# Kernel optimization log

Measured on AMD Instinct MI355X. Metric: run time of the kernel, lower is better.

## Reference

```python
import jax, jax.numpy as jnp
import numpy as np


def setup_inputs() -> dict:
    key = jax.random.key(0)
    ks = jax.random.split(key, 7)
    B, T, C, D = 8, 2048, 1024, 128
    x = jax.random.normal(ks[0], (B, T, C), dtype=jnp.float32)
    # torch nn.Linear weights are [out_features, in_features]
    s = 1.0 / np.sqrt(C)
    Wq = jax.random.normal(ks[1], (D, C), dtype=jnp.float32) * s
    bq = jax.random.normal(ks[2], (D,), dtype=jnp.float32) * s
    Wk = jax.random.normal(ks[3], (D, C), dtype=jnp.float32) * s
    bk = jax.random.normal(ks[4], (D,), dtype=jnp.float32) * s
    Wv = jax.random.normal(ks[5], (D, C), dtype=jnp.float32) * s
    bv = jax.random.normal(ks[6], (D,), dtype=jnp.float32) * s
    return {"x": x, "Wq": Wq, "bq": bq, "Wk": Wk, "bk": bk, "Wv": Wv, "bv": bv}


def reference(x, Wq, bq, Wk, bk, Wv, bv):
    B, T, C = x.shape
    q = jnp.einsum('btc,dc->btd', x, Wq) + bq  # [B,T,D]
    k = jnp.einsum('btc,dc->btd', x, Wk) + bk
    v = jnp.einsum('btc,dc->btd', x, Wv) + bv
    scores = jnp.einsum('btd,bsd->bts', q, k)  # [B,T,T]
    causal = jnp.tril(jnp.ones((T, T), dtype=bool))
    masked = jnp.where(causal, scores, -jnp.inf)
    # NOTE: original scales by sqrt(key.weight.shape[-1]) == sqrt(emb_dim), AFTER masking
    scale = jnp.asarray(C, dtype=x.dtype) ** 0.5
    attn = jax.nn.softmax(masked / scale, axis=-1)
    return jnp.einsum('bts,bsd->btd', attn, v)
```

## Files before the change

kernel.cpp:

```cpp
#include <hip/hip_runtime.h>
#include <hip/hip_bf16.h>
#include <math.h>

typedef __bf16 bf16_t;
typedef __bf16 bf16x4 __attribute__((ext_vector_type(4)));
typedef __bf16 bf16x8 __attribute__((ext_vector_type(8)));
typedef float  f32x4  __attribute__((ext_vector_type(4)));
typedef float  f32x16 __attribute__((ext_vector_type(16)));
typedef int    v2i    __attribute__((ext_vector_type(2)));

static constexpr int Bz = 8, Tt = 2048, Cc = 1024, Dd = 128;
static constexpr int Mm = Bz * Tt;
static constexpr int NT128 = Tt / 128;

__device__ __forceinline__ bf16x8 lds_read8(const char* base, int byte) {
    return *(const bf16x8*)(base + byte);
}

__device__ __forceinline__ bf16x8 cvt8(float4 a, float4 b) {
    bf16x8 r;
    r[0] = (bf16_t)a.x; r[1] = (bf16_t)a.y; r[2] = (bf16_t)a.z; r[3] = (bf16_t)a.w;
    r[4] = (bf16_t)b.x; r[5] = (bf16_t)b.y; r[6] = (bf16_t)b.z; r[7] = (bf16_t)b.w;
    return r;
}

__device__ __forceinline__ unsigned cvtpk(float lo, float hi) {
    unsigned r;
    asm("v_cvt_pk_bf16_f32 %0, %1, %2" : "=v"(r) : "v"(lo), "v"(hi));
    return r;
}

__global__ __launch_bounds__(256) void wcvt_kernel(
    const float* __restrict__ Wq, const float* __restrict__ Wk,
    const float* __restrict__ Wv, bf16_t* __restrict__ Wp)
{
    int g = (blockIdx.x * 256 + threadIdx.x) * 4;
    int n = g >> 10;
    int k = g & 1023;
    int sel = n >> 7;
    const float* W = (sel == 0) ? Wq : (sel == 1) ? Wk : Wv;
    float4 f = *(const float4*)(W + (size_t)(n & 127) * 1024 + k);
    bf16x4 o; o[0] = (bf16_t)f.x; o[1] = (bf16_t)f.y; o[2] = (bf16_t)f.z; o[3] = (bf16_t)f.w;
    int ktile = k >> 6, kk = (k >> 5) & 1, hi = (k >> 3) & 3, e = k & 7;
    int addr = (((((ktile * 24 + (n >> 4)) * 2 + kk) * 4 + hi) * 16 + (n & 15)) * 8) + e;
    *(bf16x4*)(Wp + addr) = o;
}

__global__ __launch_bounds__(256) void qkv_fused(
    const float* __restrict__ x, const bf16_t* __restrict__ Wp,
    const float* __restrict__ bq, const float* __restrict__ bk, const float* __restrict__ bv,
    bf16_t* __restrict__ qo, bf16_t* __restrict__ ko, bf16_t* __restrict__ vTo)
{
    const int m0   = blockIdx.x * 32;
    const int tid  = threadIdx.x;
    const int lane = tid & 63;
    const int w    = tid >> 6;
    const int lo   = lane & 15;
    const int hi   = lane >> 4;

    __shared__ bf16_t Xs[2][32 * 64];

    f32x4 zero4 = {0.f, 0.f, 0.f, 0.f};
    f32x4 acc[2][6];
    #pragma unroll
    for (int i = 0; i < 2; i++)
        #pragma unroll
        for (int j = 0; j < 6; j++) acc[i][j] = zero4;

    const int xrow = tid >> 3;
    const int xcol = (tid & 7) * 8;

    float4 fx[2];
    auto load_x = [&](int k0) {
        const float4* s = (const float4*)(x + (size_t)(m0 + xrow) * Cc + k0 + xcol);
        fx[0] = s[0]; fx[1] = s[1];
    };
    auto write_x = [&](int buf) {
        int byte = (xrow * 128 + xcol * 2) ^ ((xrow & 7) << 4);
        *(bf16x8*)((char*)Xs[buf] + byte) = cvt8(fx[0], fx[1]);
    };

    bf16x8 bfrA[2][6], bfrB[2][6];
    auto loadB = [&](bf16x8 (&dst)[2][6], int k0) {
        const bf16_t* base = Wp + (size_t)(k0 >> 6) * (24 * 2 * 64 * 8) + lane * 8;
        #pragma unroll
        for (int j = 0; j < 6; j++)
            #pragma unroll
            for (int kk = 0; kk < 2; kk++)
                dst[kk][j] = *(const bf16x8*)(base + (((w * 6 + j) * 2 + kk) * 64) * 8);
    };
    auto mfma_step = [&](const bf16x8 (&bfr)[2][6], int buf) {
        #pragma unroll
        for (int kk = 0; kk < 2; kk++) {
            bf16x8 af0 = lds_read8((char*)Xs[buf], ((lo)      * 128 + kk * 64 + hi * 16) ^ ((lo & 7) << 4));
            bf16x8 af1 = lds_read8((char*)Xs[buf], ((16 + lo) * 128 + kk * 64 + hi * 16) ^ ((lo & 7) << 4));
            #pragma unroll
            for (int j = 0; j < 6; j++)
                acc[0][j] = __builtin_amdgcn_mfma_f32_16x16x32_bf16(af0, bfr[kk][j], acc[0][j], 0, 0, 0);
            #pragma unroll
            for (int j = 0; j < 6; j++)
                acc[1][j] = __builtin_amdgcn_mfma_f32_16x16x32_bf16(af1, bfr[kk][j], acc[1][j], 0, 0, 0);
        }
    };

    load_x(0); write_x(0); loadB(bfrA, 0);
    __syncthreads();
    load_x(64); loadB(bfrB, 64);

    for (int k0 = 0; k0 < Cc; k0 += 128) {
        const bool m2 = (k0 + 128 < Cc);
        mfma_step(bfrA, 0);
        write_x(1);
        if (m2) load_x(k0 + 128);
        __syncthreads();
        if (m2) loadB(bfrA, k0 + 128);
        mfma_step(bfrB, 1);
        if (m2) { write_x(0); load_x(k0 + 192); }
        __syncthreads();
        if (k0 + 192 < Cc) loadB(bfrB, k0 + 192);
    }

    #pragma unroll
    for (int j = 0; j < 6; j++) {
        int c = w * 96 + j * 16 + lo;
        int t = c >> 7, d = c & 127;
        const float* bp = (t == 0) ? bq : (t == 1) ? bk : bv;
        float bb = bp[d];
        #pragma unroll
        for (int i = 0; i < 2; i++)
            #pragma unroll
            for (int r = 0; r < 4; r++) {
                int m = m0 + i * 16 + hi * 4 + r;
                float v = acc[i][j][r] + bb;
                if (t == 0)      qo[(size_t)m * Dd + d] = (bf16_t)v;
                else if (t == 1) ko[(size_t)m * Dd + d] = (bf16_t)v;
                else             vTo[(size_t)d * Mm + m] = (bf16_t)v;
            }
    }
}

__global__ __launch_bounds__(256, 2) void attn_kernel(
    const bf16_t* __restrict__ qi, const bf16_t* __restrict__ ki,
    const bf16_t* __restrict__ vTi,
    float* __restrict__ Opart, float* __restrict__ Mpart, float* __restrict__ Lpart,
    int nsplit)
{
    const int g   = blockIdx.x;
    const int per = nsplit * 8;
    const int qt  = (NT128 - 1) - g / per;
    const int rem = g % per;
    const int s   = rem >> 3;
    const int b   = rem & 7;
    const int nt  = 2 * qt + 2;
    const int t_lo = (s * nt) / nsplit;
    const int t_hi = ((s + 1) * nt) / nsplit;

    const int q0   = qt * 128;
    const int tid  = threadIdx.x;
    const int lane = tid & 63;
    const int w    = tid >> 6;
    const int rq   = lane & 31;
    const int dh   = lane >> 5;

    float* Ob = Opart + ((size_t)s * Mm + (size_t)b * Tt + q0) * Dd;
    float* Mb = Mpart + (size_t)s * Mm + (size_t)b * Tt + q0;
    float* Lb = Lpart + (size_t)s * Mm + (size_t)b * Tt + q0;

    if (t_lo >= t_hi) {
        float4 z = {0.f, 0.f, 0.f, 0.f};
        #pragma unroll
        for (int i = 0; i < 16; i++)
            ((float4*)Ob)[i * 256 + tid] = z;
        if (tid < 128) { Mb[tid] = -INFINITY; Lb[tid] = 0.f; }
        return;
    }

    __shared__ __align__(16) char smem[65536];

    const float SCALE = 1.4426950408889634f / 32.0f;
    const int qg = q0 + w * 32 + rq;
    const int qwmax = q0 + w * 32 + 31;

    bf16x8 qf[8];
    {
        const bf16_t* qrow = qi + (size_t)(b * Tt + qg) * Dd;
        #pragma unroll
        for (int ks = 0; ks < 8; ks++)
            qf[ks] = *(const bf16x8*)(qrow + ks * 16 + dh * 8);
    }

    f32x16 accO[4];
    #pragma unroll
    for (int ds = 0; ds < 4; ds++)
        #pragma unroll
        for (int e = 0; e < 16; e++) accO[ds][e] = 0.f;
    float mrun = -INFINITY, lrun = 0.f;

    const int krow = tid >> 2;
    const int kcol = (tid & 3) * 32;
    const int vrow = tid >> 1;
    const int vcol = (tid & 1) * 32;

    bf16x8 kr[4], vr[4];
    auto load_kv = [&](int t) {
        const int kv0 = t * 64;
        const bf16_t* ksrc = ki + (size_t)(b * Tt + kv0 + krow) * Dd + kcol;
        #pragma unroll
        for (int i = 0; i < 4; i++) kr[i] = *(const bf16x8*)(ksrc + i * 8);
        const bf16_t* vsrc = vTi + (size_t)vrow * Mm + (b * Tt + kv0 + vcol);
        #pragma unroll
        for (int i = 0; i < 4; i++) vr[i] = *(const bf16x8*)(vsrc + i * 8);
    };
    auto write_kv = [&](int buf) {
        char* Ksb = smem + buf * 16384;
        char* Vsb = smem + 32768 + buf * 16384;
        #pragma unroll
        for (int i = 0; i < 4; i++) {
            int byte = (krow * 256 + (kcol + i * 8) * 2) ^ ((krow & 15) << 4);
            *(bf16x8*)(Ksb + byte) = kr[i];
        }
        const int vlr = vrow & 63;
        const int vlc = (vrow >> 6) * 64 + vcol;
        #pragma unroll
        for (int i = 0; i < 4; i++) {
            int byte = (vlr * 256 + (vlc + i * 8) * 2) ^ ((vlr & 15) << 4);
            *(bf16x8*)(Vsb + byte) = vr[i];
        }
    };

    load_kv(t_lo);
    write_kv(0);
    int buf = 0;

    for (int t = t_lo; t < t_hi; t++) {
        const int kv0 = t * 64;
        const bool more = (t + 1 < t_hi);
        __syncthreads();
        if (more) load_kv(t + 1);

        if (kv0 <= qwmax) {
            const char* Ksb = smem + buf * 16384;
            const char* Vsb = smem + 32768 + buf * 16384;

            f32x16 accS0, accS1;
            #pragma unroll
            for (int e = 0; e < 16; e++) { accS0[e] = 0.f; accS1[e] = 0.f; }
            #pragma unroll
            for (int ks = 0; ks < 8; ks++) {
                int colb = (ks * 16 + dh * 8) * 2;
                bf16x8 kf0 = lds_read8(Ksb, ((rq)      * 256 + colb) ^ ((rq & 15) << 4));
                bf16x8 kf1 = lds_read8(Ksb, ((32 + rq) * 256 + colb) ^ ((rq & 15) << 4));
                accS0 = __builtin_amdgcn_mfma_f32_32x32x16_bf16(kf0, qf[ks], accS0, 0, 0, 0);
                accS1 = __builtin_amdgcn_mfma_f32_32x32x16_bf16(kf1, qf[ks], accS1, 0, 0, 0);
            }

            float pl[32];
            #pragma unroll
            for (int e = 0; e < 16; e++) {
                pl[e]      = accS0[e] * SCALE;
                pl[16 + e] = accS1[e] * SCALE;
            }
            if (kv0 + 63 > qg) {
                #pragma unroll
                for (int e = 0; e < 16; e++) {
                    int kg = kv0 + 8 * (e >> 2) + (e & 3) + 4 * dh;
                    if (kg > qg)      pl[e]      = -INFINITY;
                    if (kg + 32 > qg) pl[16 + e] = -INFINITY;
                }
            }

            float mt = pl[0];
            #pragma unroll
            for (int e = 1; e < 32; e++) mt = fmaxf(mt, pl[e]);
            mt = fmaxf(mt, __shfl_xor(mt, 32, 64));
            float mnew = fmaxf(mrun, mt);
            float muse = (mnew == -INFINITY) ? 0.f : mnew;
            float alpha = exp2f(mrun - muse);
            mrun = mnew;
            float ps = 0.f;
            #pragma unroll
            for (int e = 0; e < 32; e++) {
                float pv = exp2f(pl[e] - muse);
                pl[e] = pv;
                ps += pv;
            }
            lrun = alpha * lrun + ps;
            #pragma unroll
            for (int ds = 0; ds < 4; ds++)
                #pragma unroll
                for (int e = 0; e < 16; e++) accO[ds][e] *= alpha;

            unsigned u0[8], u1[8];
            #pragma unroll
            for (int gg = 0; gg < 8; gg++) {
                u0[gg] = cvtpk(pl[4 * gg + 0], pl[4 * gg + 1]);
                u1[gg] = cvtpk(pl[4 * gg + 2], pl[4 * gg + 3]);
            }
            bf16x8 pa[4];
            #pragma unroll
            for (int ks = 0; ks < 4; ks++) {
                v2i rA = __builtin_amdgcn_permlane32_swap((int)u0[2 * ks], (int)u0[2 * ks + 1], false, false);
                v2i rB = __builtin_amdgcn_permlane32_swap((int)u1[2 * ks], (int)u1[2 * ks + 1], false, false);
                union { unsigned wd[4]; bf16x8 v; } pu;
                pu.wd[0] = (unsigned)rA[0];
                pu.wd[1] = (unsigned)rB[0];
                pu.wd[2] = (unsigned)rA[1];
                pu.wd[3] = (unsigned)rB[1];
                pa[ks] = pu.v;
            }

            #pragma unroll
            for (int ds = 0; ds < 4; ds++) {
                int row  = (ds & 1) * 32 + rq;
                int cb   = (ds >> 1) * 64;
                #pragma unroll
                for (int ks = 0; ks < 4; ks++) {
                    int colb = (cb + ks * 16 + dh * 8) * 2;
                    bf16x8 vf = lds_read8(Vsb, (row * 256 + colb) ^ ((row & 15) << 4));
                    accO[ds] = __builtin_amdgcn_mfma_f32_32x32x16_bf16(vf, pa[ks], accO[ds], 0, 0, 0);
                }
            }
        }

        __syncthreads();
        if (more) write_kv(buf ^ 1);
        buf ^= 1;
    }

    __syncthreads();

    lrun += __shfl_xor(lrun, 32, 64);

    char* slab = smem + w * 8192;
    #pragma unroll
    for (int half = 0; half < 2; half++) {
        #pragma unroll
        for (int dsl = 0; dsl < 2; dsl++) {
            #pragma unroll
            for (int e = 0; e < 16; e++) {
                int d = 8 * (e >> 2) + (e & 3) + 4 * dh + 32 * dsl;
                int byte = (rq * 256 + d * 4) ^ ((rq & 15) << 4);
                *(float*)(slab + byte) = accO[half * 2 + dsl][e];
            }
        }
        __builtin_amdgcn_s_waitcnt(0);
        #pragma unroll
        for (int i = 0; i < 8; i++) {
            int dd = 32 * dh + 4 * i;
            int byte = (rq * 256 + dd * 4) ^ ((rq & 15) << 4);
            float4 val = *(float4*)(slab + byte);
            *(float4*)(Ob + (size_t)(w * 32 + rq) * Dd + half * 64 + dd) = val;
        }
        __builtin_amdgcn_s_waitcnt(0);
    }

    if (lane < 32) {
        Mb[w * 32 + rq] = mrun;
        Lb[w * 32 + rq] = lrun;
    }
}

__global__ __launch_bounds__(256) void combine_kernel(
    const float* __restrict__ Opart, const float* __restrict__ Mpart,
    const float* __restrict__ Lpart, float* __restrict__ out, int nsplit)
{
    int t   = blockIdx.x * 256 + threadIdx.x;
    int row = t >> 5;
    int dq  = (t & 31) << 2;
    float M = -INFINITY;
    for (int s = 0; s < nsplit; s++)
        M = fmaxf(M, Mpart[(size_t)s * Mm + row]);
    float L = 0.f;
    float o0 = 0.f, o1 = 0.f, o2 = 0.f, o3 = 0.f;
    for (int s = 0; s < nsplit; s++) {
        float ms = Mpart[(size_t)s * Mm + row];
        float ws = (ms == -INFINITY) ? 0.f : exp2f(ms - M);
        L += ws * Lpart[(size_t)s * Mm + row];
        float4 p = *(const float4*)(Opart + ((size_t)s * Mm + row) * Dd + dq);
        o0 += ws * p.x; o1 += ws * p.y; o2 += ws * p.z; o3 += ws * p.w;
    }
    float inv = 1.0f / L;
    float4 r; r.x = o0 * inv; r.y = o1 * inv; r.z = o2 * inv; r.w = o3 * inv;
    *(float4*)(out + (size_t)row * Dd + dq) = r;
}

extern "C" void kernel_launch(void* const* d_in, const int* in_sizes, int n_in,
                              void* d_out, int out_size, void* d_ws, size_t ws_size,
                              hipStream_t stream)
{
    const float* x  = (const float*)d_in[0];
    const float* Wq = (const float*)d_in[1];
    const float* bq = (const float*)d_in[2];
    const float* Wk = (const float*)d_in[3];
    const float* bk = (const float*)d_in[4];
    const float* Wv = (const float*)d_in[5];
    const float* bv = (const float*)d_in[6];
    float* out = (float*)d_out;

    bf16_t* qb = (bf16_t*)d_ws;
    bf16_t* kb = qb + (size_t)Mm * Dd;
    bf16_t* vT = kb + (size_t)Mm * Dd;
    bf16_t* Wp = vT + (size_t)Mm * Dd;
    char* p = (char*)(Wp + (size_t)384 * Cc);

    auto need = [&](int ns) {
        return (size_t)3 * Mm * Dd * 2 + (size_t)384 * Cc * 2
             + (size_t)ns * Mm * Dd * 4 + (size_t)ns * Mm * 8;
    };
    int nsplit = 4;
    while (nsplit > 1 && need(nsplit) > ws_size) nsplit >>= 1;

    float* Opart = (float*)p;
    float* Mpart = (float*)(p + (size_t)nsplit * Mm * Dd * 4);
    float* Lpart = Mpart + (size_t)nsplit * Mm;

    wcvt_kernel<<<dim3(384), 256, 0, stream>>>(Wq, Wk, Wv, Wp);
    qkv_fused<<<dim3(Mm / 32), 256, 0, stream>>>(x, Wp, bq, bk, bv, qb, kb, vT);
    attn_kernel<<<dim3(NT128 * nsplit * Bz), 256, 0, stream>>>(qb, kb, vT, Opart, Mpart, Lpart, nsplit);
    combine_kernel<<<dim3(Mm * 32 / 256), 256, 0, stream>>>(Opart, Mpart, Lpart, out, nsplit);
}
```

Measured before the change: 70.40 us.

## Retile QKV projection GEMM with LDS-staged weights via direct global-to-LDS loads

Restructures the QKV projection kernel: each block now covers 64 rows and half of the 384 output columns (2D grid, 512 threads), and it stages weight tiles into double-buffered LDS using global_load_lds. Previously every wave loaded its B fragments straight from global into registers. The weight packing layout changes to match the column-group split. This cuts redundant per-wave weight traffic and register pressure so that more rows share each weight load. The cost is more LDS use and a single sync per k-step, which could limit overlap.

```diff
diff --git a/kernel.cpp b/kernel.cpp
--- a/kernel.cpp
+++ b/kernel.cpp
@@ -28,6 +28,13 @@
     unsigned r;
     asm("v_cvt_pk_bf16_f32 %0, %1, %2" : "=v"(r) : "v"(lo), "v"(hi));
     return r;
+}
+
+typedef const __attribute__((address_space(1))) unsigned int* as1_u32p;
+typedef __attribute__((address_space(3))) unsigned int* as3_u32p;
+
+__device__ __forceinline__ void gload_lds16(const bf16_t* g, bf16_t* l) {
+    __builtin_amdgcn_global_load_lds((as1_u32p)(const void*)g, (as3_u32p)(void*)l, 16, 0, 0);
 }
 
 __global__ __launch_bounds__(256) void wcvt_kernel(
@@ -42,99 +49,97 @@
     float4 f = *(const float4*)(W + (size_t)(n & 127) * 1024 + k);
     bf16x4 o; o[0] = (bf16_t)f.x; o[1] = (bf16_t)f.y; o[2] = (bf16_t)f.z; o[3] = (bf16_t)f.w;
     int ktile = k >> 6, kk = (k >> 5) & 1, hi = (k >> 3) & 3, e = k & 7;
-    int addr = (((((ktile * 24 + (n >> 4)) * 2 + kk) * 4 + hi) * 16 + (n & 15)) * 8) + e;
+    int ng = n >> 4, cg = ng / 12, ngl = ng % 12, lo = n & 15;
+    size_t addr = (size_t)(((((ktile * 2 + cg) * 12 + ngl) * 2 + kk) * 4 + hi) * 16 + lo) * 8 + e;
     *(bf16x4*)(Wp + addr) = o;
 }
 
-__global__ __launch_bounds__(256) void qkv_fused(
+__global__ __launch_bounds__(512, 4) void qkv_fused(
     const float* __restrict__ x, const bf16_t* __restrict__ Wp,
     const float* __restrict__ bq, const float* __restrict__ bk, const float* __restrict__ bv,
     bf16_t* __restrict__ qo, bf16_t* __restrict__ ko, bf16_t* __restrict__ vTo)
 {
-    const int m0   = blockIdx.x * 32;
-    const int tid  = threadIdx.x;
+    const int m0  = blockIdx.x * 64;
+    const int cg  = blockIdx.y;
+    const int tid = threadIdx.x;
     const int lane = tid & 63;
-    const int w    = tid >> 6;
-    const int lo   = lane & 15;
-    const int hi   = lane >> 4;
-
-    __shared__ bf16_t Xs[2][32 * 64];
+    const int wv  = tid >> 6;
+    const int wr  = wv >> 2;
+    const int cw  = wv & 3;
+    const int lo  = lane & 15;
+    const int hi  = lane >> 4;
+
+    __shared__ bf16_t Wl[2][12 * 2 * 512];
+    __shared__ bf16_t Xs[2][64 * 64];
 
     f32x4 zero4 = {0.f, 0.f, 0.f, 0.f};
-    f32x4 acc[2][6];
+    f32x4 acc[2][3];
     #pragma unroll
     for (int i = 0; i < 2; i++)
         #pragma unroll
-        for (int j = 0; j < 6; j++) acc[i][j] = zero4;
+        for (int j = 0; j < 3; j++) acc[i][j] = zero4;
 
     const int xrow = tid >> 3;
     const int xcol = (tid & 7) * 8;
 
     float4 fx[2];
-    auto load_x = [&](int k0) {
-        const float4* s = (const float4*)(x + (size_t)(m0 + xrow) * Cc + k0 + xcol);
+    auto load_x = [&](int t) {
+        const float4* s = (const float4*)(x + (size_t)(m0 + xrow) * Cc + t * 64 + xcol);
         fx[0] = s[0]; fx[1] = s[1];
     };
     auto write_x = [&](int buf) {
         int byte = (xrow * 128 + xcol * 2) ^ ((xrow & 7) << 4);
         *(bf16x8*)((char*)Xs[buf] + byte) = cvt8(fx[0], fx[1]);
     };
-
-    bf16x8 bfrA[2][6], bfrB[2][6];
-    auto loadB = [&](bf16x8 (&dst)[2][6], int k0) {
-        const bf16_t* base = Wp + (size_t)(k0 >> 6) * (24 * 2 * 64 * 8) + lane * 8;
-        #pragma unroll
-        for (int j = 0; j < 6; j++)
-            #pragma unroll
-            for (int kk = 0; kk < 2; kk++)
-                dst[kk][j] = *(const bf16x8*)(base + (((w * 6 + j) * 2 + kk) * 64) * 8);
-    };
-    auto mfma_step = [&](const bf16x8 (&bfr)[2][6], int buf) {
+    auto stage_W = [&](int buf, int t) {
+        const bf16_t* base = Wp + (size_t)(t * 2 + cg) * 12288;
+        #pragma unroll
+        for (int i = 0; i < 3; i++) {
+            int c = i * 8 + wv;
+            gload_lds16(base + c * 512 + lane * 8, Wl[buf] + c * 512);
+        }
+    };
+
+    stage_W(0, 0); load_x(0); write_x(0);
+    __syncthreads();
+
+    for (int t = 0; t < 16; t++) {
+        const int buf = t & 1;
+        const bool more = (t < 15);
+        if (more) { stage_W(buf ^ 1, t + 1); load_x(t + 1); }
         #pragma unroll
         for (int kk = 0; kk < 2; kk++) {
-            bf16x8 af0 = lds_read8((char*)Xs[buf], ((lo)      * 128 + kk * 64 + hi * 16) ^ ((lo & 7) << 4));
-            bf16x8 af1 = lds_read8((char*)Xs[buf], ((16 + lo) * 128 + kk * 64 + hi * 16) ^ ((lo & 7) << 4));
-            #pragma unroll
-            for (int j = 0; j < 6; j++)
-                acc[0][j] = __builtin_amdgcn_mfma_f32_16x16x32_bf16(af0, bfr[kk][j], acc[0][j], 0, 0, 0);
-            #pragma unroll
-            for (int j = 0; j < 6; j++)
-                acc[1][j] = __builtin_amdgcn_mfma_f32_16x16x32_bf16(af1, bfr[kk][j], acc[1][j], 0, 0, 0);
-        }
-    };
-
-    load_x(0); write_x(0); loadB(bfrA, 0);
-    __syncthreads();
-    load_x(64); loadB(bfrB, 64);
-
-    for (int k0 = 0; k0 < Cc; k0 += 128) {
-        const bool m2 = (k0 + 128 < Cc);
-        mfma_step(bfrA, 0);
-        write_x(1);
-        if (m2) load_x(k0 + 128);
+            int r0 = wr * 32 + lo;
+            int r1 = wr * 32 + 16 + lo;
+            bf16x8 af0 = lds_read8((char*)Xs[buf], (r0 * 128 + kk * 64 + hi * 16) ^ ((r0 & 7) << 4));
+            bf16x8 af1 = lds_read8((char*)Xs[buf], (r1 * 128 + kk * 64 + hi * 16) ^ ((r1 & 7) << 4));
+            #pragma unroll
+            for (int j = 0; j < 3; j++) {
+                int ngl = cw * 3 + j;
+                bf16x8 bf = *(const bf16x8*)(Wl[buf] + (ngl * 2 + kk) * 512 + lane * 8);
+                acc[0][j] = __builtin_amdgcn_mfma_f32_16x16x32_bf16(af0, bf, acc[0][j], 0, 0, 0);
+                acc[1][j] = __builtin_amdgcn_mfma_f32_16x16x32_bf16(af1, bf, acc[1][j], 0, 0, 0);
+            }
+        }
+        if (more) write_x(buf ^ 1);
         __syncthreads();
-        if (m2) loadB(bfrA, k0 + 128);
-        mfma_step(bfrB, 1);
-        if (m2) { write_x(0); load_x(k0 + 192); }
-        __syncthreads();
-        if (k0 + 192 < Cc) loadB(bfrB, k0 + 192);
     }
 
     #pragma unroll
-    for (int j = 0; j < 6; j++) {
-        int c = w * 96 + j * 16 + lo;
-        int t = c >> 7, d = c & 127;
-        const float* bp = (t == 0) ? bq : (t == 1) ? bk : bv;
+    for (int j = 0; j < 3; j++) {
+        int n = cg * 192 + cw * 48 + j * 16 + lo;
+        int tsel = n >> 7, d = n & 127;
+        const float* bp = (tsel == 0) ? bq : (tsel == 1) ? bk : bv;
         float bb = bp[d];
         #pragma unroll
         for (int i = 0; i < 2; i++)
             #pragma unroll
             for (int r = 0; r < 4; r++) {
-                int m = m0 + i * 16 + hi * 4 + r;
+                int m = m0 + wr * 32 + i * 16 + hi * 4 + r;
                 float v = acc[i][j][r] + bb;
-                if (t == 0)      qo[(size_t)m * Dd + d] = (bf16_t)v;
-                else if (t == 1) ko[(size_t)m * Dd + d] = (bf16_t)v;
-                else             vTo[(size_t)d * Mm + m] = (bf16_t)v;
+                if (tsel == 0)      qo[(size_t)m * Dd + d] = (bf16_t)v;
+                else if (tsel == 1) ko[(size_t)m * Dd + d] = (bf16_t)v;
+                else                vTo[(size_t)d * Mm + m] = (bf16_t)v;
             }
     }
 }
@@ -415,7 +420,7 @@
     float* Lpart = Mpart + (size_t)nsplit * Mm;
 
     wcvt_kernel<<<dim3(384), 256, 0, stream>>>(Wq, Wk, Wv, Wp);
-    qkv_fused<<<dim3(Mm / 32), 256, 0, stream>>>(x, Wp, bq, bk, bv, qb, kb, vT);
+    qkv_fused<<<dim3(256, 2), 512, 0, stream>>>(x, Wp, bq, bk, bv, qb, kb, vT);
     attn_kernel<<<dim3(NT128 * nsplit * Bz), 256, 0, stream>>>(qb, kb, vT, Opart, Mpart, Lpart, nsplit);
     combine_kernel<<<dim3(Mm * 32 / 256), 256, 0, stream>>>(Opart, Mpart, Lpart, out, nsplit);
 }
```

Result: no change. 71.41 us (+1.4%).
